# Optimization experiments

Measured on AMD Instinct MI355X. Metric: run time of the kernel, lower is better.

The kernel has to match this reference:

```python
import jax, jax.numpy as jnp
import numpy as np

B, T, C, H = 4, 1024, 1024, 16
D = C // H  # head dim = 64
EPS = 1e-5


def _layernorm(x, g, b):
    m = jnp.mean(x, axis=-1, keepdims=True)
    v = jnp.var(x, axis=-1, keepdims=True)
    return (x - m) / jnp.sqrt(v + EPS) * g + b


def setup_inputs() -> dict:
    key = jax.random.key(0)
    ks = jax.random.split(key, 8)
    s = 0.02  # GPT-style init scale
    w = lambda k, shp: (jax.random.normal(k, shp, jnp.float32) * s)
    return {
        "x": jax.random.normal(ks[0], (B, T, C), jnp.float32),
        "ln1_g": jnp.ones((C,), jnp.float32), "ln1_b": jnp.zeros((C,), jnp.float32),
        "wq": w(ks[1], (C, C)), "bq": jnp.zeros((C,), jnp.float32),
        "wk": w(ks[2], (C, C)), "bk": jnp.zeros((C,), jnp.float32),
        "wv": w(ks[3], (C, C)), "bv": jnp.zeros((C,), jnp.float32),
        "wo": w(ks[4], (C, C)), "bo": jnp.zeros((C,), jnp.float32),
        "ln2_g": jnp.ones((C,), jnp.float32), "ln2_b": jnp.zeros((C,), jnp.float32),
        "w1": w(ks[5], (C, 4 * C)), "b1": jnp.zeros((4 * C,), jnp.float32),
        "w2": w(ks[6], (4 * C, C)), "b2": jnp.zeros((C,), jnp.float32),
    }


def reference(x, ln1_g, ln1_b, wq, bq, wk, bk, wv, bv, wo, bo,
              ln2_g, ln2_b, w1, b1, w2, b2):
    # --- causal self-attention branch: x = x + attn(ln1(x)) ---
    h = _layernorm(x, ln1_g, ln1_b)
    q = (h @ wq + bq).reshape(B, T, H, D)
    k = (h @ wk + bk).reshape(B, T, H, D)
    v = (h @ wv + bv).reshape(B, T, H, D)
    att = jnp.einsum('bqhd,bkhd->bhqk', q, k) * (1.0 / np.sqrt(D).astype(np.float32))
    causal = jnp.tril(jnp.ones((T, T), bool))
    att = jnp.where(causal, att, -jnp.inf)
    att = jax.nn.softmax(att, axis=-1)  # dropout p=0 -> identity
    y = jnp.einsum('bhqk,bkhd->bqhd', att, v).reshape(B, T, C)
    x = x + (y @ wo + bo)
    # --- MLP branch: x = x + mlp(ln2(x)) ---
    h2 = _layernorm(x, ln2_g, ln2_b)
    m = jax.nn.gelu(h2 @ w1 + b1, approximate=False)  # torch nn.GELU default = exact erf
    x = x + (m @ w2 + b2)
    return x
```

## Files before the change

kernel.cpp:

```cpp
#include <hip/hip_runtime.h>
#include <hip/hip_bf16.h>
#include <math.h>

#define B_ 4
#define T_ 1024
#define C_ 1024
#define H_ 16
#define D_ 64
#define M_ (B_*T_)

typedef __bf16 bf16;
typedef __bf16 bf16x8 __attribute__((ext_vector_type(8)));
typedef float  f32x4  __attribute__((ext_vector_type(4)));

#define MFMA16(a, b, c) __builtin_amdgcn_mfma_f32_16x16x32_bf16((a), (b), (c), 0, 0, 0)

__device__ __forceinline__ void gload16(const void* g, void* l) {
  __builtin_amdgcn_global_load_lds((const __attribute__((address_space(1))) void*)g,
                                   (__attribute__((address_space(3))) void*)l,
                                   16, 0, 0);
}

__global__ __launch_bounds__(256) void prep_k(
    const float* __restrict__ x, const float* __restrict__ ln1g,
    const float* __restrict__ ln1b,
    const float* __restrict__ wq, const float* __restrict__ wk,
    const float* __restrict__ wv, const float* __restrict__ wo,
    const float* __restrict__ w1, const float* __restrict__ w2,
    const float* __restrict__ bq, const float* __restrict__ bk,
    const float* __restrict__ bv,
    bf16* __restrict__ WqkvT, bf16* __restrict__ WoT,
    bf16* __restrict__ W1T, bf16* __restrict__ W2T,
    bf16* __restrict__ hbuf, float* __restrict__ bqkv) {
  __shared__ float tile[64][65];
  const int blk = blockIdx.x, tid = threadIdx.x;
  if (blk < 3072) {
    const float* W; bf16* WT; int K, N, n0, k0;
    if (blk < 1024)      { const int w = blk >> 8, t = blk & 255;
                           W  = (w == 0) ? wq : (w == 1) ? wk : (w == 2) ? wv : wo;
                           WT = (w < 3) ? WqkvT + (size_t)w * 1024 * 1024 : WoT;
                           K = 1024; N = 1024; n0 = (t & 15) * 64; k0 = (t >> 4) * 64; }
    else if (blk < 2048) { const int t = blk - 1024; W = w1; WT = W1T;
                           K = 1024; N = 4096; n0 = (t & 63) * 64; k0 = (t >> 6) * 64; }
    else                 { const int t = blk - 2048; W = w2; WT = W2T;
                           K = 4096; N = 1024; n0 = (t & 15) * 64; k0 = (t >> 4) * 64; }
    const int tr = tid >> 4, tc4 = (tid & 15) * 4;
#pragma unroll
    for (int p = 0; p < 4; ++p) {
      float4 v = *(const float4*)(W + (size_t)(k0 + tr + p * 16) * N + n0 + tc4);
      tile[tr + p * 16][tc4]     = v.x;
      tile[tr + p * 16][tc4 + 1] = v.y;
      tile[tr + p * 16][tc4 + 2] = v.z;
      tile[tr + p * 16][tc4 + 3] = v.w;
    }
    __syncthreads();
    const int nr = tid >> 3, k8 = (tid & 7) * 8;
#pragma unroll
    for (int p = 0; p < 2; ++p) {
      const int n = nr + p * 32;
      bf16x8 o8;
#pragma unroll
      for (int j = 0; j < 8; ++j) o8[j] = (bf16)tile[k8 + j][n];
      *(bf16x8*)(WT + (size_t)(n0 + n) * K + k0 + k8) = o8;
    }
  } else if (blk < 7168) {
    const int row = blk - 3072;
    float4 xv = ((const float4*)(x + (size_t)row * C_))[tid];
    float s  = xv.x + xv.y + xv.z + xv.w;
    float ss = xv.x*xv.x + xv.y*xv.y + xv.z*xv.z + xv.w*xv.w;
#pragma unroll
    for (int m = 32; m; m >>= 1) { s += __shfl_xor(s, m); ss += __shfl_xor(ss, m); }
    float* red = &tile[0][0];
    const int wid = tid >> 6;
    if ((tid & 63) == 0) { red[wid] = s; red[4 + wid] = ss; }
    __syncthreads();
    s  = red[0] + red[1] + red[2] + red[3];
    ss = red[4] + red[5] + red[6] + red[7];
    const float mean = s * (1.0f / C_);
    const float var  = ss * (1.0f / C_) - mean * mean;
    const float inv  = rsqrtf(var + 1e-5f);
    float4 gv = ((const float4*)ln1g)[tid];
    float4 bv = ((const float4*)ln1b)[tid];
    bf16* o = hbuf + (size_t)row * C_ + tid * 4;
    o[0] = (bf16)((xv.x - mean) * inv * gv.x + bv.x);
    o[1] = (bf16)((xv.y - mean) * inv * gv.y + bv.y);
    o[2] = (bf16)((xv.z - mean) * inv * gv.z + bv.z);
    o[3] = (bf16)((xv.w - mean) * inv * gv.w + bv.w);
  } else {
    const int i = (blk - 7168) * 256 + tid;
    bqkv[i] = (i < 1024) ? bq[i] : ((i < 2048) ? bk[i - 1024] : bv[i - 2048]);
  }
}

__global__ __launch_bounds__(256) void ln_k(const float* __restrict__ x,
                                            const float* __restrict__ g,
                                            const float* __restrict__ b,
                                            bf16* __restrict__ out) {
  int row = blockIdx.x;
  int t = threadIdx.x;
  float4 xv = ((const float4*)(x + (size_t)row * C_))[t];
  float s  = xv.x + xv.y + xv.z + xv.w;
  float ss = xv.x*xv.x + xv.y*xv.y + xv.z*xv.z + xv.w*xv.w;
#pragma unroll
  for (int m = 32; m; m >>= 1) { s += __shfl_xor(s, m); ss += __shfl_xor(ss, m); }
  __shared__ float red[8];
  int wid = t >> 6;
  if ((t & 63) == 0) { red[wid] = s; red[4 + wid] = ss; }
  __syncthreads();
  s  = red[0] + red[1] + red[2] + red[3];
  ss = red[4] + red[5] + red[6] + red[7];
  float mean = s * (1.0f / C_);
  float var  = ss * (1.0f / C_) - mean * mean;
  float inv  = rsqrtf(var + 1e-5f);
  float4 gv = ((const float4*)g)[t];
  float4 bv = ((const float4*)b)[t];
  bf16* o = out + (size_t)row * C_ + t * 4;
  o[0] = (bf16)((xv.x - mean) * inv * gv.x + bv.x);
  o[1] = (bf16)((xv.y - mean) * inv * gv.y + bv.y);
  o[2] = (bf16)((xv.z - mean) * inv * gv.z + bv.z);
  o[3] = (bf16)((xv.w - mean) * inv * gv.w + bv.w);
}

template <int BM, int BN, int WM, int WN, int EPI>
__global__ __launch_bounds__(WM*WN*64, 4)
void gemms(const bf16* __restrict__ A, const bf16* __restrict__ BT,
           const float* __restrict__ bias, const float* __restrict__ res,
           void* __restrict__ outp, int N, int K, int gx) {
  constexpr int NT = WM * WN * 64;
  constexpr int FM = BM / WM / 16, FN = BN / WN / 16;
  constexpr int RA = BM / 32, RB = BN / 32;
  __shared__ __align__(16) bf16 smem[(BM + BN) * 64];
  bf16* sA = smem;
  bf16* sB = smem + BM * 64;
  const int tid = threadIdx.x, lane = tid & 63, wid = tid >> 6;
  const int wr = wid / WN, wc = wid % WN;

  int bid = blockIdx.x;
  const int nwg = gridDim.x;
  if (!(nwg & 7)) bid = (bid & 7) * (nwg >> 3) + (bid >> 3);
  const int bx = bid % gx, by = bid / gx;
  const size_t am0 = (size_t)bx * BM, bn0 = (size_t)by * BN;

  f32x4 acc[FM][FN];
  const f32x4 fz = {0.f, 0.f, 0.f, 0.f};
#pragma unroll
  for (int m = 0; m < FM; ++m)
#pragma unroll
    for (int n = 0; n < FN; ++n) acc[m][n] = fz;

  const int srow = tid >> 3;
  const int sg = (tid & 7) ^ (srow & 7);
  const bf16* ag = A  + (am0 + srow) * (size_t)K + sg * 8;
  const bf16* bg = BT + (bn0 + srow) * (size_t)K + sg * 8;

  const int arow = lane & 15;
  const int g0 = (((lane >> 4))     ^ (lane & 7)) * 8;
  const int g1 = (((lane >> 4) + 4) ^ (lane & 7)) * 8;
  const int nt = K >> 6;

#pragma unroll
  for (int r = 0; r < RA; ++r)
    gload16(ag + (size_t)(r * 32) * K, sA + r * 2048 + tid * 8);
#pragma unroll
  for (int r = 0; r < RB; ++r)
    gload16(bg + (size_t)(r * 32) * K, sB + r * 2048 + tid * 8);

  for (int t = 0; t < nt; ++t) {
    __syncthreads();

    const bf16* pa = sA + (wr * (BM / WM) + arow) * 64;
    const bf16* pb = sB + (wc * (BN / WN) + arow) * 64;
    bf16x8 a[FM], b[FN];
#pragma unroll
    for (int m = 0; m < FM; ++m) a[m] = *(const bf16x8*)(pa + m * 16 * 64 + g0);
#pragma unroll
    for (int n = 0; n < FN; ++n) b[n] = *(const bf16x8*)(pb + n * 16 * 64 + g0);
#pragma unroll
    for (int m = 0; m < FM; ++m)
#pragma unroll
      for (int n = 0; n < FN; ++n)
        acc[m][n] = MFMA16(a[m], b[n], acc[m][n]);
    bf16x8 a1[FM], b1[FN];
#pragma unroll
    for (int m = 0; m < FM; ++m) a1[m] = *(const bf16x8*)(pa + m * 16 * 64 + g1);
#pragma unroll
    for (int n = 0; n < FN; ++n) b1[n] = *(const bf16x8*)(pb + n * 16 * 64 + g1);

    __syncthreads();

    if (t + 1 < nt) {
#pragma unroll
      for (int r = 0; r < RA; ++r)
        gload16(ag + (size_t)(t + 1) * 64 + (size_t)(r * 32) * K,
                sA + r * 2048 + tid * 8);
#pragma unroll
      for (int r = 0; r < RB; ++r)
        gload16(bg + (size_t)(t + 1) * 64 + (size_t)(r * 32) * K,
                sB + r * 2048 + tid * 8);
    }
#pragma unroll
    for (int m = 0; m < FM; ++m)
#pragma unroll
      for (int n = 0; n < FN; ++n)
        acc[m][n] = MFMA16(a1[m], b1[n], acc[m][n]);
  }

  if constexpr (EPI != 2) {
#pragma unroll
    for (int m = 0; m < FM; ++m) {
      const int row0 = wr * (BM / WM) + m * 16 + (lane >> 4) * 4;
#pragma unroll
      for (int n = 0; n < FN; ++n) {
        const int col = wc * (BN / WN) + n * 16 + (lane & 15);
        const float bv = bias[bn0 + col];
#pragma unroll
        for (int j = 0; j < 4; ++j) {
          float v = acc[m][n][j] + bv;
          if constexpr (EPI == 1) v = 0.5f * v * (1.0f + erff(v * 0.70710678118f));
          const int rr = row0 + j;
          smem[rr * BN + (((col >> 3) ^ (rr & 7)) << 3) + (col & 7)] = (bf16)v;
        }
      }
    }
    __syncthreads();
    constexpr int GR = BN / 8;
    constexpr int SI = BM * BN / (NT * 8);
#pragma unroll
    for (int i = 0; i < SI; ++i) {
      const int idx = i * NT + tid;
      const int row = idx / GR, g = idx % GR;
      *(bf16x8*)((bf16*)outp + (am0 + row) * N + bn0 + g * 8) =
          *(const bf16x8*)(smem + row * BN + ((g ^ (row & 7)) << 3));
    }
  } else {
    constexpr int PR = BM / WM;
    float* sf = (float*)smem;
#pragma unroll
    for (int h = 0; h < WM; ++h) {
      __syncthreads();
      if (wr == h) {
#pragma unroll
        for (int m = 0; m < FM; ++m) {
          const int lr0 = m * 16 + (lane >> 4) * 4;
#pragma unroll
          for (int n = 0; n < FN; ++n) {
            const int col = wc * (BN / WN) + n * 16 + (lane & 15);
            const float bv = bias[bn0 + col];
#pragma unroll
            for (int j = 0; j < 4; ++j)
              sf[(lr0 + j) * BN + col] = acc[m][n][j] + bv;
          }
        }
      }
      __syncthreads();
      constexpr int SI = PR * BN / (NT * 4);
#pragma unroll
      for (int i = 0; i < SI; ++i) {
        const int flat = (i * NT + tid) * 4;
        const int row = flat / BN, c = flat % BN;
        const size_t gi = (am0 + h * PR + row) * N + bn0 + c;
        float4 rv = *(const float4*)(res + gi);
        float4 sv = *(const float4*)(sf + row * BN + c);
        rv.x += sv.x; rv.y += sv.y; rv.z += sv.z; rv.w += sv.w;
        *(float4*)((float*)outp + gi) = rv;
      }
    }
  }
}

__global__ __launch_bounds__(256) void attn_k(const bf16* __restrict__ Q,
                                              const bf16* __restrict__ Kb,
                                              const bf16* __restrict__ Vb,
                                              bf16* __restrict__ Y, int ld) {
  int bh = blockIdx.x;
  int b = bh >> 4, h = bh & 15;
  int qt = (int)gridDim.y - 1 - (int)blockIdx.y;
  int q0 = qt * 64;
  int tid = threadIdx.x, wid = tid >> 6, lane = tid & 63;

  __shared__ __align__(16) bf16 sK[2][64 * 64];
  __shared__ __align__(16) bf16 sVT[2][64 * 64];
  __shared__ __align__(16) bf16 sP[4][16 * 64];

  const size_t rowQ = (size_t)(b * T_ + q0 + wid * 16 + (lane & 15)) * ld + h * 64 + (lane >> 4) * 8;
  bf16x8 qf0 = *(const bf16x8*)(Q + rowQ);
  bf16x8 qf1 = *(const bf16x8*)(Q + rowQ + 32);

  float m_run[4] = {-1e30f, -1e30f, -1e30f, -1e30f};
  float l_run[4] = {0.f, 0.f, 0.f, 0.f};
  const f32x4 fz = {0.f, 0.f, 0.f, 0.f};
  f32x4 o[4];
#pragma unroll
  for (int i = 0; i < 4; ++i) o[i] = fz;

  const int kgr = (lane & 7) ^ (lane >> 3);
  const bf16* kg = Kb + (size_t)(b * T_ + wid * 16 + (lane >> 3)) * ld + h * 64 + kgr * 8;
  const int lkoff = (wid * 16) * 64;
  const bf16* vg = Vb + (size_t)(b * T_ + lane) * ld + h * 64;

  const int g0 = (((lane >> 4))     ^ (lane & 7)) * 8;
  const int g1 = (((lane >> 4) + 4) ^ (lane & 7)) * 8;

  gload16(kg,                   sK[0] + lkoff);
  gload16(kg + (size_t)8 * ld,  sK[0] + lkoff + 8 * 64);
  {
    bf16x8 v0 = *(const bf16x8*)(vg + wid * 8);
    bf16x8 v1 = *(const bf16x8*)(vg + (wid + 4) * 8);
#pragma unroll
    for (int j = 0; j < 8; ++j) {
      const int pc = ((((lane >> 3) ^ j) << 3) | (lane & 7));
      sVT[0][(wid * 8 + j) * 64 + pc]       = v0[j];
      sVT[0][((wid + 4) * 8 + j) * 64 + pc] = v1[j];
    }
  }

  for (int kt = 0; kt <= qt; ++kt) {
    const int cur = kt & 1, nxt = cur ^ 1;
    const bool pf = (kt < qt);
    __syncthreads();

    bf16x8 vn0, vn1;
    if (pf) {
      const size_t k1 = (size_t)(kt + 1) * 64;
      gload16(kg + k1 * ld,        sK[nxt] + lkoff);
      gload16(kg + (k1 + 8) * ld,  sK[nxt] + lkoff + 8 * 64);
      vn0 = *(const bf16x8*)(vg + k1 * ld + wid * 8);
      vn1 = *(const bf16x8*)(vg + k1 * ld + (wid + 4) * 8);
    }

    const int k0 = kt * 64;
    f32x4 s[4];
#pragma unroll
    for (int ni = 0; ni < 4; ++ni) {
      const bf16* kr = sK[cur] + (ni * 16 + (lane & 15)) * 64;
      bf16x8 kf0 = *(const bf16x8*)(kr + g0);
      bf16x8 kf1 = *(const bf16x8*)(kr + g1);
      f32x4 t = fz;
      t = MFMA16(qf0, kf0, t);
      t = MFMA16(qf1, kf1, t);
      s[ni] = t;
    }

    int rbase = q0 + wid * 16 + (lane >> 4) * 4;
    int cbase = k0 + (lane & 15);
    float tm[4] = {-1e30f, -1e30f, -1e30f, -1e30f};
#pragma unroll
    for (int ni = 0; ni < 4; ++ni)
#pragma unroll
      for (int j = 0; j < 4; ++j) {
        float v = s[ni][j] * 0.125f;
        if (cbase + ni * 16 > rbase + j) v = -1e30f;
        s[ni][j] = v;
        tm[j] = fmaxf(tm[j], v);
      }
#pragma unroll
    for (int j = 0; j < 4; ++j)
#pragma unroll
      for (int mk = 1; mk < 16; mk <<= 1)
        tm[j] = fmaxf(tm[j], __shfl_xor(tm[j], mk));

    float fac[4], rs[4] = {0.f, 0.f, 0.f, 0.f};
#pragma unroll
    for (int j = 0; j < 4; ++j) {
      float mn = fmaxf(m_run[j], tm[j]);
      fac[j] = __expf(m_run[j] - mn);
      m_run[j] = mn;
    }
#pragma unroll
    for (int ni = 0; ni < 4; ++ni)
#pragma unroll
      for (int j = 0; j < 4; ++j) {
        float p = __expf(s[ni][j] - m_run[j]);
        rs[j] += p;
        const int crow = (lane >> 4) * 4 + j;
        const int cg = (ni * 2 + ((lane & 15) >> 3)) ^ (crow & 7);
        sP[wid][crow * 64 + (cg << 3) + (lane & 7)] = (bf16)p;
      }
#pragma unroll
    for (int j = 0; j < 4; ++j) {
#pragma unroll
      for (int mk = 1; mk < 16; mk <<= 1)
        rs[j] += __shfl_xor(rs[j], mk);
      l_run[j] = l_run[j] * fac[j] + rs[j];
    }
#pragma unroll
    for (int df = 0; df < 4; ++df)
#pragma unroll
      for (int j = 0; j < 4; ++j)
        o[df][j] *= fac[j];

#pragma unroll
    for (int kk = 0; kk < 2; ++kk) {
      const int gk = kk ? g1 : g0;
      bf16x8 pf8 = *(const bf16x8*)(sP[wid] + (lane & 15) * 64 + gk);
#pragma unroll
      for (int df = 0; df < 4; ++df) {
        bf16x8 vf = *(const bf16x8*)(sVT[cur] + (df * 16 + (lane & 15)) * 64 + gk);
        o[df] = MFMA16(pf8, vf, o[df]);
      }
    }

    if (pf) {
#pragma unroll
      for (int j = 0; j < 8; ++j) {
        const int pc = ((((lane >> 3) ^ j) << 3) | (lane & 7));
        sVT[nxt][(wid * 8 + j) * 64 + pc]       = vn0[j];
        sVT[nxt][((wid + 4) * 8 + j) * 64 + pc] = vn1[j];
      }
    }
  }

#pragma unroll
  for (int df = 0; df < 4; ++df)
#pragma unroll
    for (int j = 0; j < 4; ++j) {
      int row = q0 + wid * 16 + (lane >> 4) * 4 + j;
      int d = df * 16 + (lane & 15);
      Y[(size_t)(b * T_ + row) * C_ + h * 64 + d] = (bf16)(o[df][j] / l_run[j]);
    }
}

extern "C" void kernel_launch(void* const* d_in, const int* in_sizes, int n_in,
                              void* d_out, int out_size, void* d_ws, size_t ws_size,
                              hipStream_t stream) {
  (void)in_sizes; (void)n_in; (void)out_size; (void)ws_size;
  const float* x    = (const float*)d_in[0];
  const float* ln1g = (const float*)d_in[1];
  const float* ln1b = (const float*)d_in[2];
  const float* wq   = (const float*)d_in[3];
  const float* bq   = (const float*)d_in[4];
  const float* wk   = (const float*)d_in[5];
  const float* bk   = (const float*)d_in[6];
  const float* wv   = (const float*)d_in[7];
  const float* bv   = (const float*)d_in[8];
  const float* wo   = (const float*)d_in[9];
  const float* bo   = (const float*)d_in[10];
  const float* ln2g = (const float*)d_in[11];
  const float* ln2b = (const float*)d_in[12];
  const float* w1   = (const float*)d_in[13];
  const float* b1   = (const float*)d_in[14];
  const float* w2   = (const float*)d_in[15];
  const float* b2   = (const float*)d_in[16];

  char* ws = (char*)d_ws;
  const size_t MB = 1024 * 1024;
  bf16* WqkvT = (bf16*)(ws +  0 * MB);
  bf16* WoT   = (bf16*)(ws +  6 * MB);
  bf16* W1T   = (bf16*)(ws +  8 * MB);
  bf16* W2T   = (bf16*)(ws + 16 * MB);
  bf16* hbuf  = (bf16*)(ws + 24 * MB);
  bf16* qkv   = (bf16*)(ws + 32 * MB);
  bf16* yb    = (bf16*)(ws + 56 * MB);
  bf16* mb    = (bf16*)(ws + 32 * MB);
  float* x1   = (float*)(ws + 64 * MB);
  float* bqkv = (float*)d_out;

  dim3 blk(256);
  prep_k<<<7180, blk, 0, stream>>>(x, ln1g, ln1b, wq, wk, wv, wo, w1, w2,
                                   bq, bk, bv, WqkvT, WoT, W1T, W2T, hbuf, bqkv);
  gemms<128,128,2,2,0><<<768,  blk, 0, stream>>>(hbuf, WqkvT, bqkv, nullptr, qkv, 3072, 1024, 32);
  attn_k<<<dim3(64, 16), blk, 0, stream>>>(qkv, qkv + 1024, qkv + 2048, yb, 3072);
  gemms<64,128,2,2,2><<<512,   blk, 0, stream>>>(yb, WoT, bo, x, x1, 1024, 1024, 64);
  ln_k<<<M_, blk, 0, stream>>>(x1, ln2g, ln2b, hbuf);
  gemms<128,128,2,2,1><<<1024, blk, 0, stream>>>(hbuf, W1T, b1, nullptr, mb, 4096, 1024, 32);
  gemms<64,128,2,2,2><<<512,   blk, 0, stream>>>(mb, W2T, b2, x1, (float*)d_out, 1024, 4096, 64);
}
```

Before: 211.3 us.

## Double-buffer GEMM LDS tiles with K-step of 32 to overlap loads

Replaces the single-buffered 64-wide K tile with two 32-wide LDS buffers. The next tile is issued into the alternate buffer right after the barrier, which drops one barrier per iteration and lets global-to-LDS loads overlap the MFMAs on the current buffer. LDS use per block stays the same, but each iteration now does half the MFMA work per barrier and the swizzle changes to 4 groups, which may bring back bank conflicts. The epilogue also needs extra space: it reuses the whole buffer and adds a barrier after the loop.

```diff
diff --git a/kernel.cpp b/kernel.cpp
--- a/kernel.cpp
+++ b/kernel.cpp
@@ -128,10 +128,8 @@
            void* __restrict__ outp, int N, int K, int gx) {
   constexpr int NT = WM * WN * 64;
   constexpr int FM = BM / WM / 16, FN = BN / WN / 16;
-  constexpr int RA = BM / 32, RB = BN / 32;
-  __shared__ __align__(16) bf16 smem[(BM + BN) * 64];
-  bf16* sA = smem;
-  bf16* sB = smem + BM * 64;
+  constexpr int RA = BM / 64, RB = BN / 64;
+  __shared__ __align__(16) bf16 smem[2][(BM + BN) * 32];
   const int tid = threadIdx.x, lane = tid & 63, wid = tid >> 6;
   const int wr = wid / WN, wc = wid % WN;
 
@@ -148,63 +146,48 @@
 #pragma unroll
     for (int n = 0; n < FN; ++n) acc[m][n] = fz;
 
-  const int srow = tid >> 3;
-  const int sg = (tid & 7) ^ (srow & 7);
-  const bf16* ag = A  + (am0 + srow) * (size_t)K + sg * 8;
-  const bf16* bg = BT + (bn0 + srow) * (size_t)K + sg * 8;
+  const int srow = tid >> 2;
+  const int sg = ((tid & 3) ^ (srow & 3)) * 8;
+  const bf16* ag = A  + (am0 + srow) * (size_t)K + sg;
+  const bf16* bg = BT + (bn0 + srow) * (size_t)K + sg;
+
+  auto stage = [&](int buf, int t) {
+#pragma unroll
+    for (int r = 0; r < RA; ++r)
+      gload16(ag + (size_t)t * 32 + (size_t)(r * 64) * K,
+              &smem[buf][r * 2048 + tid * 8]);
+#pragma unroll
+    for (int r = 0; r < RB; ++r)
+      gload16(bg + (size_t)t * 32 + (size_t)(r * 64) * K,
+              &smem[buf][BM * 32 + r * 2048 + tid * 8]);
+  };
 
   const int arow = lane & 15;
-  const int g0 = (((lane >> 4))     ^ (lane & 7)) * 8;
-  const int g1 = (((lane >> 4) + 4) ^ (lane & 7)) * 8;
-  const int nt = K >> 6;
-
-#pragma unroll
-  for (int r = 0; r < RA; ++r)
-    gload16(ag + (size_t)(r * 32) * K, sA + r * 2048 + tid * 8);
-#pragma unroll
-  for (int r = 0; r < RB; ++r)
-    gload16(bg + (size_t)(r * 32) * K, sB + r * 2048 + tid * 8);
-
+  const int gph = (((lane >> 4)) ^ (lane & 3)) * 8;
+  const int nt = K >> 5;
+
+  stage(0, 0);
   for (int t = 0; t < nt; ++t) {
+    const int cur = t & 1;
     __syncthreads();
-
-    const bf16* pa = sA + (wr * (BM / WM) + arow) * 64;
-    const bf16* pb = sB + (wc * (BN / WN) + arow) * 64;
+    if (t + 1 < nt) stage(cur ^ 1, t + 1);
+
+    const bf16* pa = &smem[cur][(wr * (BM / WM) + arow) * 32 + gph];
+    const bf16* pb = &smem[cur][BM * 32 + (wc * (BN / WN) + arow) * 32 + gph];
     bf16x8 a[FM], b[FN];
 #pragma unroll
-    for (int m = 0; m < FM; ++m) a[m] = *(const bf16x8*)(pa + m * 16 * 64 + g0);
-#pragma unroll
-    for (int n = 0; n < FN; ++n) b[n] = *(const bf16x8*)(pb + n * 16 * 64 + g0);
+    for (int m = 0; m < FM; ++m) a[m] = *(const bf16x8*)(pa + m * 16 * 32);
+#pragma unroll
+    for (int n = 0; n < FN; ++n) b[n] = *(const bf16x8*)(pb + n * 16 * 32);
 #pragma unroll
     for (int m = 0; m < FM; ++m)
 #pragma unroll
       for (int n = 0; n < FN; ++n)
         acc[m][n] = MFMA16(a[m], b[n], acc[m][n]);
-    bf16x8 a1[FM], b1[FN];
-#pragma unroll
-    for (int m = 0; m < FM; ++m) a1[m] = *(const bf16x8*)(pa + m * 16 * 64 + g1);
-#pragma unroll
-    for (int n = 0; n < FN; ++n) b1[n] = *(const bf16x8*)(pb + n * 16 * 64 + g1);
-
-    __syncthreads();
-
-    if (t + 1 < nt) {
-#pragma unroll
-      for (int r = 0; r < RA; ++r)
-        gload16(ag + (size_t)(t + 1) * 64 + (size_t)(r * 32) * K,
-                sA + r * 2048 + tid * 8);
-#pragma unroll
-      for (int r = 0; r < RB; ++r)
-        gload16(bg + (size_t)(t + 1) * 64 + (size_t)(r * 32) * K,
-                sB + r * 2048 + tid * 8);
-    }
-#pragma unroll
-    for (int m = 0; m < FM; ++m)
-#pragma unroll
-      for (int n = 0; n < FN; ++n)
-        acc[m][n] = MFMA16(a1[m], b1[n], acc[m][n]);
   }
-
+  __syncthreads();
+
+  bf16* smf = &smem[0][0];
   if constexpr (EPI != 2) {
 #pragma unroll
     for (int m = 0; m < FM; ++m) {
@@ -218,7 +201,7 @@
           float v = acc[m][n][j] + bv;
           if constexpr (EPI == 1) v = 0.5f * v * (1.0f + erff(v * 0.70710678118f));
           const int rr = row0 + j;
-          smem[rr * BN + (((col >> 3) ^ (rr & 7)) << 3) + (col & 7)] = (bf16)v;
+          smf[rr * BN + (((col >> 3) ^ (rr & 7)) << 3) + (col & 7)] = (bf16)v;
         }
       }
     }
@@ -230,11 +213,11 @@
       const int idx = i * NT + tid;
       const int row = idx / GR, g = idx % GR;
       *(bf16x8*)((bf16*)outp + (am0 + row) * N + bn0 + g * 8) =
-          *(const bf16x8*)(smem + row * BN + ((g ^ (row & 7)) << 3));
+          *(const bf16x8*)(smf + row * BN + ((g ^ (row & 7)) << 3));
     }
   } else {
     constexpr int PR = BM / WM;
-    float* sf = (float*)smem;
+    float* sf = (float*)smf;
 #pragma unroll
     for (int h = 0; h < WM; ++h) {
       __syncthreads();
```

Result: slower. 223.6 us (+5.8%).

## Split-K the W2 down-projection GEMM into two halves with a combine kernel

Applied to the files above, without the earlier changes.

The final MLP down-projection (K=4096) is split into two K halves, which doubles the grid from 512 to 1024 workgroups. The first half writes bias plus residual plus partial to the output, and the second half writes its fp32 partial to a workspace buffer. A new combine kernel then adds the partial into the output. This is meant to raise occupancy and cut per-block serial K-loop time, at the cost of an extra 16MB fp32 write/read pass and one more kernel launch. The partial buffer reuses workspace that held the transposed weights, which are no longer needed at that point.

```diff
diff --git a/kernel.cpp b/kernel.cpp
--- a/kernel.cpp
+++ b/kernel.cpp
@@ -121,11 +121,21 @@
   o[3] = (bf16)((xv.w - mean) * inv * gv.w + bv.w);
 }
 
+__global__ __launch_bounds__(256) void combine_k(float* __restrict__ out,
+                                                 const float* __restrict__ part) {
+  const size_t i = ((size_t)blockIdx.x * 256 + threadIdx.x) * 4;
+  float4 a = *(const float4*)(out + i);
+  float4 p = *(const float4*)(part + i);
+  a.x += p.x; a.y += p.y; a.z += p.z; a.w += p.w;
+  *(float4*)(out + i) = a;
+}
+
 template <int BM, int BN, int WM, int WN, int EPI>
 __global__ __launch_bounds__(WM*WN*64, 4)
 void gemms(const bf16* __restrict__ A, const bf16* __restrict__ BT,
            const float* __restrict__ bias, const float* __restrict__ res,
-           void* __restrict__ outp, int N, int K, int gx) {
+           void* __restrict__ outp, float* __restrict__ part,
+           int N, int Kloop, int ldk, int gx, int nby) {
   constexpr int NT = WM * WN * 64;
   constexpr int FM = BM / WM / 16, FN = BN / WN / 16;
   constexpr int RA = BM / 32, RB = BN / 32;
@@ -138,7 +148,9 @@
   int bid = blockIdx.x;
   const int nwg = gridDim.x;
   if (!(nwg & 7)) bid = (bid & 7) * (nwg >> 3) + (bid >> 3);
-  const int bx = bid % gx, by = bid / gx;
+  const int bx = bid % gx;
+  int by = bid / gx, ks = 0;
+  if (by >= nby) { ks = 1; by -= nby; }
   const size_t am0 = (size_t)bx * BM, bn0 = (size_t)by * BN;
 
   f32x4 acc[FM][FN];
@@ -150,20 +162,21 @@
 
   const int srow = tid >> 3;
   const int sg = (tid & 7) ^ (srow & 7);
-  const bf16* ag = A  + (am0 + srow) * (size_t)K + sg * 8;
-  const bf16* bg = BT + (bn0 + srow) * (size_t)K + sg * 8;
+  const size_t koff = (size_t)ks * Kloop;
+  const bf16* ag = A  + (am0 + srow) * (size_t)ldk + koff + sg * 8;
+  const bf16* bg = BT + (bn0 + srow) * (size_t)ldk + koff + sg * 8;
 
   const int arow = lane & 15;
   const int g0 = (((lane >> 4))     ^ (lane & 7)) * 8;
   const int g1 = (((lane >> 4) + 4) ^ (lane & 7)) * 8;
-  const int nt = K >> 6;
+  const int nt = Kloop >> 6;
 
 #pragma unroll
   for (int r = 0; r < RA; ++r)
-    gload16(ag + (size_t)(r * 32) * K, sA + r * 2048 + tid * 8);
+    gload16(ag + (size_t)(r * 32) * ldk, sA + r * 2048 + tid * 8);
 #pragma unroll
   for (int r = 0; r < RB; ++r)
-    gload16(bg + (size_t)(r * 32) * K, sB + r * 2048 + tid * 8);
+    gload16(bg + (size_t)(r * 32) * ldk, sB + r * 2048 + tid * 8);
 
   for (int t = 0; t < nt; ++t) {
     __syncthreads();
@@ -191,11 +204,11 @@
     if (t + 1 < nt) {
 #pragma unroll
       for (int r = 0; r < RA; ++r)
-        gload16(ag + (size_t)(t + 1) * 64 + (size_t)(r * 32) * K,
+        gload16(ag + (size_t)(t + 1) * 64 + (size_t)(r * 32) * ldk,
                 sA + r * 2048 + tid * 8);
 #pragma unroll
       for (int r = 0; r < RB; ++r)
-        gload16(bg + (size_t)(t + 1) * 64 + (size_t)(r * 32) * K,
+        gload16(bg + (size_t)(t + 1) * 64 + (size_t)(r * 32) * ldk,
                 sB + r * 2048 + tid * 8);
     }
 #pragma unroll
@@ -245,7 +258,7 @@
 #pragma unroll
           for (int n = 0; n < FN; ++n) {
             const int col = wc * (BN / WN) + n * 16 + (lane & 15);
-            const float bv = bias[bn0 + col];
+            const float bv = (ks == 0) ? bias[bn0 + col] : 0.f;
 #pragma unroll
             for (int j = 0; j < 4; ++j)
               sf[(lr0 + j) * BN + col] = acc[m][n][j] + bv;
@@ -259,10 +272,14 @@
         const int flat = (i * NT + tid) * 4;
         const int row = flat / BN, c = flat % BN;
         const size_t gi = (am0 + h * PR + row) * N + bn0 + c;
-        float4 rv = *(const float4*)(res + gi);
         float4 sv = *(const float4*)(sf + row * BN + c);
-        rv.x += sv.x; rv.y += sv.y; rv.z += sv.z; rv.w += sv.w;
-        *(float4*)((float*)outp + gi) = rv;
+        if (ks == 0) {
+          float4 rv = *(const float4*)(res + gi);
+          rv.x += sv.x; rv.y += sv.y; rv.z += sv.z; rv.w += sv.w;
+          *(float4*)((float*)outp + gi) = rv;
+        } else {
+          *(float4*)(part + gi) = sv;
+        }
       }
     }
   }
@@ -453,15 +470,18 @@
   bf16* yb    = (bf16*)(ws + 56 * MB);
   bf16* mb    = (bf16*)(ws + 32 * MB);
   float* x1   = (float*)(ws + 64 * MB);
+  float* part = (float*)(ws +  0 * MB);
   float* bqkv = (float*)d_out;
+  const int BIG = 1 << 20;
 
   dim3 blk(256);
   prep_k<<<7180, blk, 0, stream>>>(x, ln1g, ln1b, wq, wk, wv, wo, w1, w2,
                                    bq, bk, bv, WqkvT, WoT, W1T, W2T, hbuf, bqkv);
-  gemms<128,128,2,2,0><<<768,  blk, 0, stream>>>(hbuf, WqkvT, bqkv, nullptr, qkv, 3072, 1024, 32);
+  gemms<128,128,2,2,0><<<768,  blk, 0, stream>>>(hbuf, WqkvT, bqkv, nullptr, qkv, nullptr, 3072, 1024, 1024, 32, BIG);
   attn_k<<<dim3(64, 16), blk, 0, stream>>>(qkv, qkv + 1024, qkv + 2048, yb, 3072);
-  gemms<64,128,2,2,2><<<512,   blk, 0, stream>>>(yb, WoT, bo, x, x1, 1024, 1024, 64);
+  gemms<64,128,2,2,2><<<512,   blk, 0, stream>>>(yb, WoT, bo, x, x1, nullptr, 1024, 1024, 1024, 64, BIG);
   ln_k<<<M_, blk, 0, stream>>>(x1, ln2g, ln2b, hbuf);
-  gemms<128,128,2,2,1><<<1024, blk, 0, stream>>>(hbuf, W1T, b1, nullptr, mb, 4096, 1024, 32);
-  gemms<64,128,2,2,2><<<512,   blk, 0, stream>>>(mb, W2T, b2, x1, (float*)d_out, 1024, 4096, 64);
-}
+  gemms<128,128,2,2,1><<<1024, blk, 0, stream>>>(hbuf, W1T, b1, nullptr, mb, nullptr, 4096, 1024, 1024, 32, BIG);
+  gemms<64,128,2,2,2><<<1024,  blk, 0, stream>>>(mb, W2T, b2, x1, (float*)d_out, part, 1024, 2048, 4096, 64, 8);
+  combine_k<<<4096, blk, 0, stream>>>((float*)d_out, part);
+}
```

Result: no change. 214.5 us (+1.5%).
